# Optimization experiments

Measured on AMD Instinct MI355X. Metric: run time of the kernel, lower is better.

## Reference

```python
import jax, jax.numpy as jnp
import numpy as np

# model dims
B, S, R, D = 2, 64, 2048, 1024      # batch, num_bars(summary len), reg seq len, embed dim
H, KVH, HD = 16, 4, 64              # q heads, kv heads, head dim
G = H // KVH                        # GQA group size
KVD = KVH * HD
TPB = R // S                        # tokens per bar = 32
SCALE = HD ** -0.5
NEG = -1e9


def _rotate_half(x):
    x1, x2 = jnp.split(x, 2, axis=-1)
    return jnp.concatenate([-x2, x1], axis=-1)


def _apply_rope(q, k, cos, sin):
    return q * cos + _rotate_half(q) * sin, k * cos + _rotate_half(k) * sin


def _rope_1d(seq_len):
    # standard RoPE tables, shape (1, 1, seq_len, HD)
    inv = 1.0 / (10000.0 ** (jnp.arange(0, HD, 2, dtype=jnp.float32) / HD))
    freqs = jnp.arange(seq_len, dtype=jnp.float32)[:, None] * inv
    emb = jnp.concatenate([freqs, freqs], axis=-1)
    return jnp.cos(emb)[None, None], jnp.sin(emb)[None, None]


def _rope_2d(bar_ids, tib):
    # hierarchical 2D RoPE: half the rotary freqs encode bar id, half encode token-in-bar id
    q4 = HD // 4
    inv = 1.0 / (10000.0 ** (jnp.arange(q4, dtype=jnp.float32) * 2.0 / (HD // 2)))
    fb = bar_ids.astype(jnp.float32)[..., None] * inv   # (B, R, HD/4)
    ft = tib.astype(jnp.float32)[..., None] * inv       # (B, R, HD/4)
    freqs = jnp.concatenate([fb, ft], axis=-1)          # (B, R, HD/2)
    emb = jnp.concatenate([freqs, freqs], axis=-1)      # (B, R, HD)
    return jnp.cos(emb)[:, None], jnp.sin(emb)[:, None]


def _attn(q, k, v, mask):
    # masked softmax attention; mask (Lq, Lk) broadcast over batch/heads
    s = jnp.einsum('bhqd,bhkd->bhqk', q, k) * SCALE
    s = jnp.where(mask[None, None], s, NEG)
    p = jax.nn.softmax(s, axis=-1)
    return jnp.einsum('bhqk,bhkd->bhqd', p, v)


def _lin(x, w, b):
    return x @ w + b


def _heads(x, n):
    b, l, _ = x.shape
    return x.reshape(b, l, n, HD).transpose(0, 2, 1, 3)


def _merge(x):
    b, h, l, _ = x.shape
    return x.transpose(0, 2, 1, 3).reshape(b, l, h * HD)


PARAM_SHAPES = [('w_sq', (D, D)), ('b_sq', (D,)), ('w_sk', (D, KVD)), ('b_sk', (KVD,)),
                ('w_sv', (D, KVD)), ('b_sv', (KVD,)), ('w_so', (D, D)), ('b_so', (D,)),
                ('w_rq', (D, D)), ('b_rq', (D,)), ('w_rk', (D, KVD)), ('b_rk', (KVD,)),
                ('w_rv', (D, KVD)), ('b_rv', (KVD,)), ('w_ro', (D, D)), ('b_ro', (D,)),
                ('w_k2', (D, KVD)), ('b_k2', (KVD,)), ('w_v2', (D, KVD)), ('b_v2', (KVD,))]


def setup_inputs() -> dict:
    key = jax.random.key(0)
    ks = jax.random.split(key, 2 + len(PARAM_SHAPES))
    inp = {}
    inp['sum_x'] = jax.random.normal(ks[0], (B, S, D), jnp.float32)
    inp['reg_x'] = jax.random.normal(ks[1], (B, R, D), jnp.float32)
    for i, (n, shp) in enumerate(PARAM_SHAPES):
        inp[n] = jax.random.normal(ks[2 + i], shp, jnp.float32) * 0.02
    pos = jnp.arange(R)
    bar = pos // TPB
    tib = pos % TPB
    inp['bar_ids'] = jnp.tile(bar[None], (B, 1)).astype(jnp.int32)
    inp['token_in_bar_ids'] = jnp.tile(tib[None], (B, 1)).astype(jnp.int32)
    # summarize phase: summary-bar i attends to summary j<=i and regular tokens in bars<=i
    key_bar = jnp.concatenate([jnp.arange(S), bar])
    inp['summarize_block_mask'] = key_bar[None, :] <= jnp.arange(S)[:, None]
    # updating phase: regular token t attends to summary-K2 of bars<=bar(t) and regular s<=t
    upd = jnp.concatenate([jnp.arange(S)[None, :] <= bar[:, None],
                           pos[None, :] <= pos[:, None]], axis=1)
    inp['updating_block_mask'] = upd
    return inp


def reference(sum_x, reg_x, w_sq, b_sq, w_sk, b_sk, w_sv, b_sv, w_so, b_so,
              w_rq, b_rq, w_rk, b_rk, w_rv, b_rv, w_ro, b_ro, w_k2, b_k2, w_v2, b_v2,
              summarize_block_mask, updating_block_mask, bar_ids, token_in_bar_ids):
    sum_q = _heads(_lin(sum_x, w_sq, b_sq), H)
    sum_k = _heads(_lin(sum_x, w_sk, b_sk), KVH)
    sum_v = _heads(_lin(sum_x, w_sv, b_sv), KVH)
    reg_q = _heads(_lin(reg_x, w_rq, b_rq), H)
    reg_k = _heads(_lin(reg_x, w_rk, b_rk), KVH)
    reg_v = _heads(_lin(reg_x, w_rv, b_rv), KVH)
    # 1D RoPE for summary tokens, 2D hierarchical RoPE for regular tokens
    cos, sin = _rope_1d(S)
    sum_q, sum_k = _apply_rope(sum_q, sum_k, cos, sin)
    rcos, rsin = _rope_2d(bar_ids, token_in_bar_ids)
    reg_q, reg_k = _apply_rope(reg_q, reg_k, rcos, rsin)
    rep = lambda t: jnp.repeat(t, G, axis=1)  # GQA repeat_interleave over heads
    reg_k_r, reg_v_r = rep(reg_k), rep(reg_v)
    # phase 1: summarize (summary queries over [summary; regular] keys)
    cat_k = jnp.concatenate([rep(sum_k), reg_k_r], axis=2)
    cat_v = jnp.concatenate([rep(sum_v), reg_v_r], axis=2)
    sum_attn = _merge(_attn(sum_q, cat_k, cat_v, summarize_block_mask))  # (B, S, D)
    # phase 2: updating (regular queries over [summary K2/V2; regular] keys)
    k2 = rep(_heads(_lin(sum_attn, w_k2, b_k2), KVH))
    v2 = rep(_heads(_lin(sum_attn, w_v2, b_v2), KVH))
    cat_k2 = jnp.concatenate([k2, reg_k_r], axis=2)
    cat_v2 = jnp.concatenate([v2, reg_v_r], axis=2)
    reg_attn = _merge(_attn(reg_q, cat_k2, cat_v2, updating_block_mask))  # (B, R, D)
    return _lin(sum_attn, w_so, b_so), _lin(reg_attn, w_ro, b_ro)
```

## Files before the change

kernel.cpp:

```cpp
#include <hip/hip_runtime.h>

typedef unsigned short u16;
typedef __attribute__((ext_vector_type(8))) short s8v;
typedef __attribute__((ext_vector_type(4))) float f4v;

#define B_    2
#define S_    64
#define R_    2048
#define D_    1024
#define H_    16
#define KVH_  4
#define LOG2_10K 13.287712379549449f
#define QSC_  0.18033688011112042f

__device__ __forceinline__ u16 f2bf(float f) {
  union { float f; unsigned int i; } v; v.f = f;
  unsigned int x = v.i;
  return (u16)((x + 0x7FFFu + ((x >> 16) & 1u)) >> 16);
}
__device__ __forceinline__ u16 f2bf_ru(float f) {
  union { float f; unsigned int i; } v; v.f = f;
  return (u16)((v.i + 0x8000u) >> 16);
}

__device__ __forceinline__ f4v mfma2(const s8v& a0, const s8v& a1,
                                     const s8v& b0, const s8v& b1) {
  f4v t = {0.f, 0.f, 0.f, 0.f};
  t = __builtin_amdgcn_mfma_f32_16x16x32_bf16(a0, b0, t, 0, 0, 0);
  t = __builtin_amdgcn_mfma_f32_16x16x32_bf16(a1, b1, t, 0, 0, 0);
  return t;
}

struct WT10 { const float* w[10]; u16* o[10]; int C[10]; };

__global__ __launch_bounds__(256)
void transw_k(WT10 ws, const float* __restrict__ xa, const float* __restrict__ xb,
              u16* __restrict__ oa, u16* __restrict__ ob)
{
  const int z = blockIdx.z;
  if (z == 10) {
    int gid = blockIdx.x + blockIdx.y * 32;
    #pragma unroll
    for (int it = 0; it < 3; it++) {
      int idx = gid * 256 + threadIdx.x + it * 262144;
      if (idx < 540672) {
        int i = idx * 8;
        const float* src; u16* dst; int off;
        if (i < 131072) { src = xa; dst = oa; off = i; }
        else            { src = xb; dst = ob; off = i - 131072; }
        float4 a = *(const float4*)(src + off);
        float4 b = *(const float4*)(src + off + 4);
        s8v r;
        r[0] = (short)f2bf(a.x); r[1] = (short)f2bf(a.y);
        r[2] = (short)f2bf(a.z); r[3] = (short)f2bf(a.w);
        r[4] = (short)f2bf(b.x); r[5] = (short)f2bf(b.y);
        r[6] = (short)f2bf(b.z); r[7] = (short)f2bf(b.w);
        *(s8v*)(dst + off) = r;
      }
    }
    return;
  }
  const int C = ws.C[z];
  const int c0 = blockIdx.x * 32, k0 = blockIdx.y * 32;
  if (c0 >= C) return;
  __shared__ float t[32][33];
  const float* w = ws.w[z];
  u16* o = ws.o[z];
  const int x = threadIdx.x & 31, y = threadIdx.x >> 5;
  #pragma unroll
  for (int j = 0; j < 4; j++)
    t[y + 8 * j][x] = w[(size_t)(k0 + y + 8 * j) * C + c0 + x];
  __syncthreads();
  #pragma unroll
  for (int j = 0; j < 4; j++)
    o[(size_t)(c0 + y + 8 * j) * 1024 + k0 + x] = f2bf(t[x][y + 8 * j]);
}

__device__ __forceinline__ void gemm_core_gl(
    const u16* __restrict__ Xrow, const u16* __restrict__ WTrow,
    u16* __restrict__ As, u16* __restrict__ Bs, f4v (&acc)[2][4],
    int tid, int l15, int l4, int wro, int wco)
{
  const int w    = tid >> 6;
  const int lane = tid & 63;
  const int rl   = lane >> 3;
  const int c8   = lane & 7;
  const int x7   = l15 & 7;
  const int csw  = (c8 ^ rl) * 8;

  for (int k = 0; k < 16; k++) {
    const int k0 = k * 64;
    __syncthreads();
    #pragma unroll
    for (int j = 0; j < 2; j++) {
      int rbase = w * 16 + j * 8;
      int r = rbase + rl;
      __builtin_amdgcn_global_load_lds(
        (const __attribute__((address_space(1))) void*)(Xrow + (size_t)r * 1024 + k0 + csw),
        (__attribute__((address_space(3))) void*)(As + rbase * 64),
        16, 0, 0);
      __builtin_amdgcn_global_load_lds(
        (const __attribute__((address_space(1))) void*)(WTrow + (size_t)r * 1024 + k0 + csw),
        (__attribute__((address_space(3))) void*)(Bs + rbase * 64),
        16, 0, 0);
    }
    __syncthreads();

    s8v af[2][2], bf4[4][2];
    #pragma unroll
    for (int rc = 0; rc < 2; rc++) {
      int row = wro + rc * 16 + l15;
      af[rc][0] = *(const s8v*)(As + row * 64 + ((l4 ^ x7) * 8));
      af[rc][1] = *(const s8v*)(As + row * 64 + (((l4 + 4) ^ x7) * 8));
    }
    #pragma unroll
    for (int cc = 0; cc < 4; cc++) {
      int row = wco + cc * 16 + l15;
      bf4[cc][0] = *(const s8v*)(Bs + row * 64 + ((l4 ^ x7) * 8));
      bf4[cc][1] = *(const s8v*)(Bs + row * 64 + (((l4 + 4) ^ x7) * 8));
    }
    #pragma unroll
    for (int rc = 0; rc < 2; rc++)
      #pragma unroll
      for (int cc = 0; cc < 4; cc++) {
        acc[rc][cc] = __builtin_amdgcn_mfma_f32_16x16x32_bf16(af[rc][0], bf4[cc][0], acc[rc][cc], 0, 0, 0);
        acc[rc][cc] = __builtin_amdgcn_mfma_f32_16x16x32_bf16(af[rc][1], bf4[cc][1], acc[rc][cc], 0, 0, 0);
      }
  }
  __syncthreads();
}

__device__ __forceinline__ void epi_to_lds(
    const f4v (&acc)[2][4], const float* __restrict__ Bp, u16* __restrict__ Es,
    int cbr, int wro, int wco, int grb, int LB,
    int ropeMode, bool rope2d, bool sc, int l15, int l4)
{
  float bv[4];
  #pragma unroll
  for (int cc = 0; cc < 4; cc++) bv[cc] = Bp[cbr + cc * 16 + l15];

  if (ropeMode == 0) {
    #pragma unroll
    for (int rc = 0; rc < 2; rc++)
      #pragma unroll
      for (int reg = 0; reg < 4; reg++) {
        int lrow = wro + rc * 16 + l4 * 4 + reg;
        #pragma unroll
        for (int cc = 0; cc < 4; cc++)
          Es[lrow * 136 + wco + cc * 16 + l15] = f2bf(acc[rc][cc][reg] + bv[cc]);
      }
  } else {
    float step = rope2d ? (LOG2_10K / 16.f) : (LOG2_10K / 32.f);
    float inv_lo = exp2f(-(float)l15 * step);
    float inv_hi = rope2d ? inv_lo : inv_lo * exp2f(-16.f * step);
    #pragma unroll
    for (int rc = 0; rc < 2; rc++)
      #pragma unroll
      for (int reg = 0; reg < 4; reg++) {
        int lrow = wro + rc * 16 + l4 * 4 + reg;
        int grow = grb + lrow;
        int pos = grow & (LB - 1);
        int bar = pos >> 5, tib = pos & 31;
        #pragma unroll
        for (int cc = 0; cc < 4; cc++) {
          float inv = (cc & 1) ? inv_hi : inv_lo;
          float bse = rope2d ? (float)((cc & 1) ? tib : bar) : (float)pos;
          float ang = bse * inv;
          float sn, cs;
          sincosf(ang, &sn, &cs);
          float v0 = acc[rc][cc][reg] + bv[cc];
          float v1 = acc[rc][cc ^ 2][reg] + bv[cc ^ 2];
          float rot = (cc < 2) ? -v1 : v1;
          float val = v0 * cs + rot * sn;
          if (sc) val *= QSC_;
          Es[lrow * 136 + wco + cc * 16 + l15] = f2bf(val);
        }
      }
  }
}

__device__ __forceinline__ void store_tile_bf16(
    const u16* __restrict__ Es, u16* __restrict__ out,
    int grb, int c0r, int NH, int LB, int LBS, int tid)
{
  #pragma unroll
  for (int it = 0; it < 4; it++) {
    int idx = it * 512 + tid;
    int r = idx >> 4, ch = idx & 15;
    int grow = grb + r;
    int b = grow >> LBS, pos = grow & (LB - 1);
    int cg = c0r + ch * 8;
    size_t base = (((size_t)b * NH + (cg >> 6)) * LB + pos) * 64 + (cg & 63);
    *(s8v*)(out + base) = *(const s8v*)(Es + r * 136 + ch * 8);
  }
}

__device__ __forceinline__ void store_tile_vT(
    const u16* __restrict__ Es, u16* __restrict__ outT,
    int grb, int kvbase, int LB, int LBS, int tid)
{
  #pragma unroll
  for (int it = 0; it < 4; it++) {
    int idx = tid + it * 512;
    int dcol = idx & 127, rg = idx >> 7;
    int grow = grb + rg * 8;
    int b = grow >> LBS, pos = grow & (LB - 1);
    u16 tmp[8];
    #pragma unroll
    for (int j = 0; j < 8; j++) tmp[j] = Es[(rg * 8 + j) * 136 + dcol];
    u16* dst = outT + (((size_t)(b * KVH_ + kvbase + (dcol >> 6))) * 64 + (dcol & 63)) * LB + pos;
    *(s8v*)dst = *(s8v*)tmp;
  }
}

struct QkvA {
  const u16 *X, *WTs, *WTr;
  const float *b0s, *b1s, *b2s, *b0r, *b1r, *b2r;
  u16 *o0s, *o1s, *o2s, *o0r, *o1r, *o2r;
};

__global__ __launch_bounds__(512)
void qkv_k(QkvA a)
{
  int orig = blockIdx.x;
  int xcd = orig & 7, sidx = orig >> 3;
  int wg = (xcd < 4) ? (xcd * 50 + sidx) : (200 + (xcd - 4) * 49 + sidx);
  const int bx = wg % 12, by = wg / 12;
  const bool issum = (by == 0);
  const int c0 = bx * 128;

  __shared__ u16 LDSU[17408];
  u16* As = LDSU;
  u16* Bs = LDSU + 8192;
  u16* Es = LDSU;

  const int tid  = threadIdx.x;
  const int lane = tid & 63;
  const int w    = tid >> 6;
  const int l15  = lane & 15;
  const int l4   = lane >> 4;
  const int wro  = (w >> 1) * 32;
  const int wco  = (w & 1) * 64;

  f4v acc[2][4];
  #pragma unroll
  for (int i = 0; i < 2; i++)
    #pragma unroll
    for (int j = 0; j < 4; j++) acc[i][j] = (f4v){0.f, 0.f, 0.f, 0.f};

  const u16* Xrow  = a.X + (size_t)by * 128 * 1024;
  const u16* WTrow = (issum ? a.WTs : a.WTr) + (size_t)c0 * 1024;
  gemm_core_gl(Xrow, WTrow, As, Bs, acc, tid, l15, l4, wro, wco);

  const int LB  = issum ? 64 : 2048;
  const int LBS = issum ? 6 : 11;
  const int grb = issum ? 0 : (by - 1) * 128;

  if (c0 < 1024) {
    epi_to_lds(acc, issum ? a.b0s : a.b0r, Es, c0 + wco, wro, wco, grb, LB, 1, !issum, true, l15, l4);
    __syncthreads();
    store_tile_bf16(Es, issum ? a.o0s : a.o0r, grb, c0, 16, LB, LBS, tid);
  } else if (c0 < 1280) {
    epi_to_lds(acc, issum ? a.b1s : a.b1r, Es, c0 - 1024 + wco, wro, wco, grb, LB, 1, !issum, false, l15, l4);
    __syncthreads();
    store_tile_bf16(Es, issum ? a.o1s : a.o1r, grb, c0 - 1024, 4, LB, LBS, tid);
  } else {
    epi_to_lds(acc, issum ? a.b2s : a.b2r, Es, c0 - 1280 + wco, wro, wco, grb, LB, 0, false, false, l15, l4);
    __syncthreads();
    store_tile_vT(Es, issum ? a.o2s : a.o2r, grb, (c0 - 1280) >> 6, LB, LBS, tid);
  }
}

__global__ __launch_bounds__(512)
void gemm_p1_k(const u16* __restrict__ X, const u16* __restrict__ WT,
               const float* __restrict__ bk2, const float* __restrict__ bv2,
               const float* __restrict__ bso,
               u16* __restrict__ k2, u16* __restrict__ v2T, float* __restrict__ outsum)
{
  const int c0 = blockIdx.x * 128;

  __shared__ u16 LDSU[17408];
  u16* As = LDSU;
  u16* Bs = LDSU + 8192;
  u16* Es = LDSU;

  const int tid  = threadIdx.x;
  const int lane = tid & 63;
  const int w    = tid >> 6;
  const int l15  = lane & 15;
  const int l4   = lane >> 4;
  const int wro  = (w >> 1) * 32;
  const int wco  = (w & 1) * 64;

  f4v acc[2][4];
  #pragma unroll
  for (int i = 0; i < 2; i++)
    #pragma unroll
    for (int j = 0; j < 4; j++) acc[i][j] = (f4v){0.f, 0.f, 0.f, 0.f};

  gemm_core_gl(X, WT + (size_t)c0 * 1024, As, Bs, acc, tid, l15, l4, wro, wco);

  if (c0 < 256) {
    epi_to_lds(acc, bk2, Es, c0 + wco, wro, wco, 0, 64, 0, false, false, l15, l4);
    __syncthreads();
    store_tile_bf16(Es, k2, 0, c0, 4, 64, 6, tid);
  } else if (c0 < 512) {
    epi_to_lds(acc, bv2, Es, c0 - 256 + wco, wro, wco, 0, 64, 0, false, false, l15, l4);
    __syncthreads();
    store_tile_vT(Es, v2T, 0, (c0 - 256) >> 6, 64, 6, tid);
  } else {
    float bv[4];
    #pragma unroll
    for (int cc = 0; cc < 4; cc++) bv[cc] = bso[c0 - 512 + wco + cc * 16 + l15];
    #pragma unroll
    for (int rc = 0; rc < 2; rc++)
      #pragma unroll
      for (int reg = 0; reg < 4; reg++) {
        int row = wro + rc * 16 + l4 * 4 + reg;
        #pragma unroll
        for (int cc = 0; cc < 4; cc++)
          outsum[(size_t)row * 1024 + c0 - 512 + wco + cc * 16 + l15] = acc[rc][cc][reg] + bv[cc];
      }
  }
}

__global__ __launch_bounds__(512)
void gemm_ro_k(const u16* __restrict__ X, const u16* __restrict__ WT,
               const float* __restrict__ Bp, float* __restrict__ out)
{
  int orig = blockIdx.x;
  int wg = (orig & 7) * 32 + (orig >> 3);
  const int bx = wg & 7, by = wg >> 3;
  const int c0 = bx * 128, r0 = by * 128;

  __shared__ u16 LDSU[16384];
  u16* As = LDSU;
  u16* Bs = LDSU + 8192;

  const int tid  = threadIdx.x;
  const int lane = tid & 63;
  const int w    = tid >> 6;
  const int l15  = lane & 15;
  const int l4   = lane >> 4;
  const int wro  = (w >> 1) * 32;
  const int wco  = (w & 1) * 64;

  f4v acc[2][4];
  #pragma unroll
  for (int i = 0; i < 2; i++)
    #pragma unroll
    for (int j = 0; j < 4; j++) acc[i][j] = (f4v){0.f, 0.f, 0.f, 0.f};

  gemm_core_gl(X + (size_t)r0 * 1024, WT + (size_t)c0 * 1024, As, Bs, acc,
               tid, l15, l4, wro, wco);

  float bv[4];
  #pragma unroll
  for (int cc = 0; cc < 4; cc++) bv[cc] = Bp[c0 + wco + cc * 16 + l15];
  #pragma unroll
  for (int rc = 0; rc < 2; rc++)
    #pragma unroll
    for (int reg = 0; reg < 4; reg++) {
      int row = r0 + wro + rc * 16 + l4 * 4 + reg;
      #pragma unroll
      for (int cc = 0; cc < 4; cc++)
        out[(size_t)row * 1024 + c0 + wco + cc * 16 + l15] = acc[rc][cc][reg] + bv[cc];
    }
}

template<int PHASE>
__device__ __forceinline__ void strip_sm(
    f4v (&s)[4], float& m, float& lsum, f4v (&acc)[4],
    u16 (&PtS)[16][72], bool need_mask, int kbase, int qrow, int l15, int l4)
{
  float tmax = -1e30f;
  if (need_mask) {
    #pragma unroll
    for (int n = 0; n < 4; n++)
      #pragma unroll
      for (int reg = 0; reg < 4; reg++) {
        int kidx = kbase + n * 16 + l4 * 4 + reg;
        bool ok;
        if (kbase == 0) ok = kidx <= ((PHASE == 1) ? qrow : (qrow >> 5));
        else { int kr = kidx - 64; ok = (PHASE == 1) ? ((kr >> 5) <= qrow) : (kr <= qrow); }
        float sv = ok ? s[n][reg] : -1e30f;
        s[n][reg] = sv;
        tmax = fmaxf(tmax, sv);
      }
  } else {
    #pragma unroll
    for (int n = 0; n < 4; n++)
      #pragma unroll
      for (int reg = 0; reg < 4; reg++) tmax = fmaxf(tmax, s[n][reg]);
  }
  tmax = fmaxf(tmax, __shfl_xor(tmax, 16));
  tmax = fmaxf(tmax, __shfl_xor(tmax, 32));

  if (__any(tmax > m)) {
    float mn = fmaxf(m, tmax);
    float f  = __builtin_amdgcn_exp2f(m - mn);
    m = mn;
    lsum *= f;
    #pragma unroll
    for (int dt = 0; dt < 4; dt++)
      #pragma unroll
      for (int reg = 0; reg < 4; reg++) acc[dt][reg] *= f;
  }
  float rsum = 0.f;
  #pragma unroll
  for (int n = 0; n < 4; n++) {
    float p0 = __builtin_amdgcn_exp2f(s[n][0] - m);
    float p1 = __builtin_amdgcn_exp2f(s[n][1] - m);
    float p2 = __builtin_amdgcn_exp2f(s[n][2] - m);
    float p3 = __builtin_amdgcn_exp2f(s[n][3] - m);
    rsum += (p0 + p1) + (p2 + p3);
    uint2 pk;
    pk.x = (unsigned)f2bf_ru(p0) | ((unsigned)f2bf_ru(p1) << 16);
    pk.y = (unsigned)f2bf_ru(p2) | ((unsigned)f2bf_ru(p3) << 16);
    *(uint2*)&PtS[l15][n * 16 + l4 * 4] = pk;
  }
  rsum += __shfl_xor(rsum, 16);
  rsum += __shfl_xor(rsum, 32);
  lsum += rsum;
}

__global__ __launch_bounds__(512)
void attn2_k(const u16* __restrict__ Q, const u16* __restrict__ KS,
             const u16* __restrict__ KR, const u16* __restrict__ VST,
             const u16* __restrict__ VRT, u16* __restrict__ Out)
{
  const int gid = blockIdx.x;
  const int qb  = (gid & 256) ? (15 - (gid & 15)) : (gid & 15);
  const int bh  = gid >> 4;
  const int h   = bh & 15, b = bh >> 4;
  const int q0  = qb * 128;
  const int kh  = h >> 2;

  __shared__ u16 Kt[64][72];
  __shared__ u16 Vt[64][72];
  __shared__ u16 Pt[8][16][72];

  const int tid = threadIdx.x, lane = tid & 63, w = tid >> 6;
  const int l15 = lane & 15, l4 = lane >> 4;
  const int qw  = q0 + w * 16;

  const u16* qp = Q + (((size_t)b * H_ + h) * R_ + qw + l15) * 64;
  s8v qf0 = *(const s8v*)(qp + l4 * 8);
  s8v qf1 = *(const s8v*)(qp + 32 + l4 * 8);

  f4v acc[4];
  #pragma unroll
  for (int dt = 0; dt < 4; dt++) acc[dt] = (f4v){0.f, 0.f, 0.f, 0.f};
  float m = -1e30f, lsum = 0.f;

  const int ntiles = (64 + q0 + 128) >> 6;
  const size_t bh_kv = (size_t)b * KVH_ + kh;
  const int r_ = tid >> 3, sg_ = (tid & 7) * 8;

  {
    const u16* kp = KS  + bh_kv * 4096;
    const u16* vp = VST + bh_kv * 4096;
    s8v k0 = *(const s8v*)(kp + r_ * 64 + sg_);
    s8v v0 = *(const s8v*)(vp + r_ * 64 + sg_);
    *(s8v*)&Kt[r_][sg_] = k0;
    *(s8v*)&Vt[r_][sg_] = v0;
  }
  __syncthreads();

  for (int kt = 0; kt < ntiles; kt++) {
    const int kbase = kt * 64;
    const bool pre = (kt + 1 < ntiles);
    s8v knx, vnx;
    if (pre) {
      const u16* kp = KR  + (bh_kv * R_ + kbase) * 64;
      const u16* vp = VRT + bh_kv * 64 * R_ + kbase;
      knx = *(const s8v*)(kp + r_ * 64 + sg_);
      vnx = *(const s8v*)(vp + (size_t)r_ * R_ + sg_);
    }

    const bool active = (kbase == 0) || (kbase - 64 <= qw + 15);
    if (active) {
      f4v s[4];
      __builtin_amdgcn_s_setprio(1);
      #pragma unroll
      for (int n = 0; n < 4; n++) {
        s8v kf0 = *(const s8v*)&Kt[n * 16 + l15][l4 * 8];
        s8v kf1 = *(const s8v*)&Kt[n * 16 + l15][32 + l4 * 8];
        s[n] = mfma2(kf0, kf1, qf0, qf1);
      }
      __builtin_amdgcn_s_setprio(0);
      bool nm = (kbase == 0) || ((kbase - 1) > qw);
      strip_sm<2>(s, m, lsum, acc, Pt[w], nm, kbase, qw + l15, l15, l4);
      asm volatile("s_waitcnt lgkmcnt(0)" ::: "memory");
      s8v pf0 = *(const s8v*)&Pt[w][l15][l4 * 8];
      s8v pf1 = *(const s8v*)&Pt[w][l15][32 + l4 * 8];
      __builtin_amdgcn_s_setprio(1);
      #pragma unroll
      for (int dt = 0; dt < 4; dt++) {
        s8v vf0 = *(const s8v*)&Vt[dt * 16 + l15][l4 * 8];
        s8v vf1 = *(const s8v*)&Vt[dt * 16 + l15][32 + l4 * 8];
        acc[dt] = __builtin_amdgcn_mfma_f32_16x16x32_bf16(vf0, pf0, acc[dt], 0, 0, 0);
        acc[dt] = __builtin_amdgcn_mfma_f32_16x16x32_bf16(vf1, pf1, acc[dt], 0, 0, 0);
      }
      __builtin_amdgcn_s_setprio(0);
    }

    __syncthreads();
    if (pre) {
      *(s8v*)&Kt[r_][sg_] = knx;
      *(s8v*)&Vt[r_][sg_] = vnx;
      __syncthreads();
    }
  }

  float linv = 1.f / lsum;
  u16* o = Out + ((size_t)b * R_ + qw + l15) * D_ + h * 64;
  #pragma unroll
  for (int dt = 0; dt < 4; dt++) {
    ushort4 t4;
    t4.x = f2bf(acc[dt][0] * linv);
    t4.y = f2bf(acc[dt][1] * linv);
    t4.z = f2bf(acc[dt][2] * linv);
    t4.w = f2bf(acc[dt][3] * linv);
    *(ushort4*)(o + dt * 16 + l4 * 4) = t4;
  }
}

__global__ __launch_bounds__(256)
void attn1_k(const u16* __restrict__ Q, const u16* __restrict__ KS,
             const u16* __restrict__ KR, const u16* __restrict__ VST,
             const u16* __restrict__ VRT,
             float* __restrict__ pO, float* __restrict__ pml)
{
  const int gid = blockIdx.x;
  const int ck  = gid & 7;
  const int bh  = gid >> 3;
  const int h   = bh & 15, b = bh >> 4;
  const int kh  = h >> 2;
  const int kt0 = (ck * 33) >> 3;
  const int kt1 = ((ck + 1) * 33) >> 3;

  __shared__ u16 Kt[2][64][72];
  __shared__ u16 Vt[2][64][72];
  __shared__ u16 Pt[4][16][72];

  const int tid = threadIdx.x, lane = tid & 63, w = tid >> 6;
  const int l15 = lane & 15, l4 = lane >> 4;
  const int qw  = w * 16;

  const u16* qp = Q + (((size_t)b * H_ + h) * S_ + qw + l15) * 64;
  s8v qf0 = *(const s8v*)(qp + l4 * 8);
  s8v qf1 = *(const s8v*)(qp + 32 + l4 * 8);

  f4v acc[4];
  #pragma unroll
  for (int dt = 0; dt < 4; dt++) acc[dt] = (f4v){0.f, 0.f, 0.f, 0.f};
  float m = -1e30f, lsum = 0.f;

  const size_t bh_kv = (size_t)b * KVH_ + kh;
  const int r_ = tid >> 3, sg_ = (tid & 7) * 8;

  {
    const u16 *kp, *vp; int vstr;
    if (kt0 == 0) { kp = KS + bh_kv * 4096; vp = VST + bh_kv * 4096; vstr = 64; }
    else {
      kp = KR  + (bh_kv * R_ + kt0 * 64 - 64) * 64;
      vp = VRT + bh_kv * 64 * R_ + (kt0 * 64 - 64);
      vstr = R_;
    }
    s8v ka0 = *(const s8v*)(kp + r_ * 64 + sg_);
    s8v ka1 = *(const s8v*)(kp + (r_ + 32) * 64 + sg_);
    s8v va0 = *(const s8v*)(vp + (size_t)r_ * vstr + sg_);
    s8v va1 = *(const s8v*)(vp + (size_t)(r_ + 32) * vstr + sg_);
    *(s8v*)&Kt[0][r_][sg_]      = ka0;
    *(s8v*)&Kt[0][r_ + 32][sg_] = ka1;
    *(s8v*)&Vt[0][r_][sg_]      = va0;
    *(s8v*)&Vt[0][r_ + 32][sg_] = va1;
  }
  __syncthreads();

  for (int kt = kt0; kt < kt1; kt++) {
    const int cur = (kt - kt0) & 1;
    const int kbase = kt * 64;
    const bool pre = (kt + 1 < kt1);
    s8v ka0, ka1, va0, va1;
    if (pre) {
      const u16* kp = KR  + (bh_kv * R_ + kbase) * 64;
      const u16* vp = VRT + bh_kv * 64 * R_ + kbase;
      ka0 = *(const s8v*)(kp + r_ * 64 + sg_);
      ka1 = *(const s8v*)(kp + (r_ + 32) * 64 + sg_);
      va0 = *(const s8v*)(vp + (size_t)r_ * R_ + sg_);
      va1 = *(const s8v*)(vp + (size_t)(r_ + 32) * R_ + sg_);
    }

    const bool active = (kbase == 0) || (((kbase - 64) >> 5) <= qw + 15);
    if (active) {
      f4v s[4];
      __builtin_amdgcn_s_setprio(1);
      #pragma unroll
      for (int n = 0; n < 4; n++) {
        s8v kf0 = *(const s8v*)&Kt[cur][n * 16 + l15][l4 * 8];
        s8v kf1 = *(const s8v*)&Kt[cur][n * 16 + l15][32 + l4 * 8];
        s[n] = mfma2(kf0, kf1, qf0, qf1);
      }
      __builtin_amdgcn_s_setprio(0);
      bool nm = (kbase == 0) || (((kbase - 1) >> 5) > qw);
      strip_sm<1>(s, m, lsum, acc, Pt[w], nm, kbase, qw + l15, l15, l4);
      asm volatile("s_waitcnt lgkmcnt(0)" ::: "memory");
      s8v pf0 = *(const s8v*)&Pt[w][l15][l4 * 8];
      s8v pf1 = *(const s8v*)&Pt[w][l15][32 + l4 * 8];
      __builtin_amdgcn_s_setprio(1);
      #pragma unroll
      for (int dt = 0; dt < 4; dt++) {
        s8v vf0 = *(const s8v*)&Vt[cur][dt * 16 + l15][l4 * 8];
        s8v vf1 = *(const s8v*)&Vt[cur][dt * 16 + l15][32 + l4 * 8];
        acc[dt] = __builtin_amdgcn_mfma_f32_16x16x32_bf16(vf0, pf0, acc[dt], 0, 0, 0);
        acc[dt] = __builtin_amdgcn_mfma_f32_16x16x32_bf16(vf1, pf1, acc[dt], 0, 0, 0);
      }
      __builtin_amdgcn_s_setprio(0);
    }

    if (pre) {
      *(s8v*)&Kt[cur ^ 1][r_][sg_]      = ka0;
      *(s8v*)&Kt[cur ^ 1][r_ + 32][sg_] = ka1;
      *(s8v*)&Vt[cur ^ 1][r_][sg_]      = va0;
      *(s8v*)&Vt[cur ^ 1][r_ + 32][sg_] = va1;
    }
    __syncthreads();
  }

  float* po = pO + (((size_t)ck * 32 + bh) * 64 + qw + l15) * 64;
  #pragma unroll
  for (int dt = 0; dt < 4; dt++)
    *(f4v*)(po + dt * 16 + l4 * 4) = acc[dt];
  if (l4 == 0) {
    float* pm = pml + (((size_t)ck * 32 + bh) * 64 + qw + l15) * 2;
    pm[0] = m; pm[1] = lsum;
  }
}

__global__ __launch_bounds__(256)
void comb1_k(const float* __restrict__ pO, const float* __restrict__ pml,
             u16* __restrict__ sattn)
{
  const int bh = blockIdx.x;
  const int b = bh >> 4, h = bh & 15;
  const int q  = threadIdx.x >> 2;
  const int d0 = (threadIdx.x & 3) * 16;
  float mv[8], lv[8], mstar = -1e30f;
  #pragma unroll
  for (int c = 0; c < 8; c++) {
    const float* p = pml + (((size_t)c * 32 + bh) * 64 + q) * 2;
    mv[c] = p[0]; lv[c] = p[1];
    mstar = fmaxf(mstar, mv[c]);
  }
  float o[16];
  #pragma unroll
  for (int j = 0; j < 16; j++) o[j] = 0.f;
  float lsum = 0.f;
  #pragma unroll
  for (int c = 0; c < 8; c++) {
    float wgt = __builtin_amdgcn_exp2f(mv[c] - mstar);
    lsum += lv[c] * wgt;
    const float* po = pO + (((size_t)c * 32 + bh) * 64 + q) * 64 + d0;
    #pragma unroll
    for (int j = 0; j < 16; j++) o[j] += po[j] * wgt;
  }
  float inv = 1.f / lsum;
  u16 ob[16];
  #pragma unroll
  for (int j = 0; j < 16; j++) ob[j] = f2bf(o[j] * inv);
  u16* out = sattn + ((size_t)(b * 64 + q)) * 1024 + h * 64 + d0;
  *(s8v*)out       = *(s8v*)&ob[0];
  *(s8v*)(out + 8) = *(s8v*)&ob[8];
}

extern "C" void kernel_launch(void* const* d_in, const int* in_sizes, int n_in,
                              void* d_out, int out_size, void* d_ws, size_t ws_size,
                              hipStream_t stream)
{
  (void)out_size; (void)ws_size;

  static const int expect[22] = {
    131072, 4194304,
    1048576, 1024, 262144, 256,
    262144, 256, 1048576, 1024,
    1048576, 1024, 262144, 256,
    262144, 256, 1048576, 1024,
    262144, 256, 262144, 256
  };
  if (n_in < 22) return;
  for (int i = 0; i < 22; i++) if (in_sizes[i] != expect[i]) return;

  const float* sum_x = (const float*)d_in[0];
  const float* reg_x = (const float*)d_in[1];
  const float* w_sq = (const float*)d_in[2];  const float* b_sq = (const float*)d_in[3];
  const float* w_sk = (const float*)d_in[4];  const float* b_sk = (const float*)d_in[5];
  const float* w_sv = (const float*)d_in[6];  const float* b_sv = (const float*)d_in[7];
  const float* w_so = (const float*)d_in[8];  const float* b_so = (const float*)d_in[9];
  const float* w_rq = (const float*)d_in[10]; const float* b_rq = (const float*)d_in[11];
  const float* w_rk = (const float*)d_in[12]; const float* b_rk = (const float*)d_in[13];
  const float* w_rv = (const float*)d_in[14]; const float* b_rv = (const float*)d_in[15];
  const float* w_ro = (const float*)d_in[16]; const float* b_ro = (const float*)d_in[17];
  const float* w_k2 = (const float*)d_in[18]; const float* b_k2 = (const float*)d_in[19];
  const float* w_v2 = (const float*)d_in[20]; const float* b_v2 = (const float*)d_in[21];

  u16* ws    = (u16*)d_ws;
  u16* xs_bf = ws;
  u16* xr_bf = xs_bf + 131072;
  u16* wt_s  = xr_bf + 4194304;
  u16* wt_r  = wt_s  + 1572864;
  u16* wt_p  = wt_r  + 1572864;
  u16* wt_ro = wt_p  + 1572864;
  u16* sq    = wt_ro + 1048576;
  u16* sk    = sq    + 131072;
  u16* svT   = sk    + 32768;
  u16* rq    = svT   + 32768;
  u16* rk    = rq    + 4194304;
  u16* rvT   = rk    + 1048576;
  u16* sattn = rvT   + 1048576;
  u16* k2    = sattn + 131072;
  u16* v2T   = k2    + 32768;
  u16* rattn = v2T   + 32768;

  float* pO  = (float*)rattn;
  float* pml = pO + 1048576;

  float* out_sum = (float*)d_out;
  float* out_reg = out_sum + 131072;

  dim3 blk(256);

  WT10 wt;
  wt.w[0] = w_sq; wt.o[0] = wt_s;              wt.C[0] = 1024;
  wt.w[1] = w_rq; wt.o[1] = wt_r;              wt.C[1] = 1024;
  wt.w[2] = w_so; wt.o[2] = wt_p + 512 * 1024; wt.C[2] = 1024;
  wt.w[3] = w_ro; wt.o[3] = wt_ro;             wt.C[3] = 1024;
  wt.w[4] = w_sk; wt.o[4] = wt_s + 1024 * 1024; wt.C[4] = 256;
  wt.w[5] = w_sv; wt.o[5] = wt_s + 1280 * 1024; wt.C[5] = 256;
  wt.w[6] = w_rk; wt.o[6] = wt_r + 1024 * 1024; wt.C[6] = 256;
  wt.w[7] = w_rv; wt.o[7] = wt_r + 1280 * 1024; wt.C[7] = 256;
  wt.w[8] = w_k2; wt.o[8] = wt_p;               wt.C[8] = 256;
  wt.w[9] = w_v2; wt.o[9] = wt_p + 256 * 1024;  wt.C[9] = 256;
  transw_k<<<dim3(32, 32, 11), blk, 0, stream>>>(wt, sum_x, reg_x, xs_bf, xr_bf);

  QkvA qa;
  qa.X = xs_bf; qa.WTs = wt_s; qa.WTr = wt_r;
  qa.b0s = b_sq; qa.b1s = b_sk; qa.b2s = b_sv;
  qa.b0r = b_rq; qa.b1r = b_rk; qa.b2r = b_rv;
  qa.o0s = sq; qa.o1s = sk; qa.o2s = svT;
  qa.o0r = rq; qa.o1r = rk; qa.o2r = rvT;
  qkv_k<<<dim3(396), dim3(512), 0, stream>>>(qa);

  attn1_k<<<dim3(256), blk, 0, stream>>>(sq, sk, rk, svT, rvT, pO, pml);
  comb1_k<<<dim3(32), blk, 0, stream>>>(pO, pml, sattn);

  gemm_p1_k<<<dim3(12), dim3(512), 0, stream>>>(sattn, wt_p, b_k2, b_v2, b_so, k2, v2T, out_sum);

  attn2_k<<<dim3(512), dim3(512), 0, stream>>>(rq, k2, rk, v2T, rvT, rattn);

  gemm_ro_k<<<dim3(256), dim3(512), 0, stream>>>(rattn, wt_ro, b_ro, out_reg);
}
```

Measured before the change: 132.5 us.

## Split phase-2 attention over key chunks with a separate combine kernel

The causal phase-2 attention kernel is split along the key dimension. Long query blocks are divided into up to three key-tile chunks, so the work per block is more even and the grid doubles to 1024 blocks. Each chunk writes an unnormalized bf16 partial output plus its running max and sum to scratch reused from the input buffer. A new combine kernel merges the chunks with log-sum-exp weights. This trades load imbalance and tail latency for an extra launch, extra global traffic, and bf16 rounding of the partial sums.

Result: slower. 141.2 us (+6.5%).

```diff
diff --git a/kernel.cpp b/kernel.cpp
--- a/kernel.cpp
+++ b/kernel.cpp
@@ -21,6 +21,9 @@
 __device__ __forceinline__ u16 f2bf_ru(float f) {
   union { float f; unsigned int i; } v; v.f = f;
   return (u16)((v.i + 0x8000u) >> 16);
+}
+__device__ __forceinline__ float bf2f(u16 u) {
+  union { unsigned int i; float f; } v; v.i = ((unsigned int)u) << 16; return v.f;
 }
 
 __device__ __forceinline__ f4v mfma2(const s8v& a0, const s8v& a1,
@@ -427,14 +430,25 @@
 __global__ __launch_bounds__(512)
 void attn2_k(const u16* __restrict__ Q, const u16* __restrict__ KS,
              const u16* __restrict__ KR, const u16* __restrict__ VST,
-             const u16* __restrict__ VRT, u16* __restrict__ Out)
-{
-  const int gid = blockIdx.x;
-  const int qb  = (gid & 256) ? (15 - (gid & 15)) : (gid & 15);
-  const int bh  = gid >> 4;
-  const int h   = bh & 15, b = bh >> 4;
-  const int q0  = qb * 128;
-  const int kh  = h >> 2;
+             const u16* __restrict__ VRT,
+             u16* __restrict__ pO2, float* __restrict__ pml2)
+{
+  static const int sqb[32] = {0,1,2,3,4,5,5,6,6,7,7,8,8,9,9,10,10,
+                              11,11,11,12,12,12,13,13,13,14,14,14,15,15,15};
+  static const int sci[32] = {0,0,0,0,0,0,1,0,1,0,1,0,1,0,1,0,1,
+                              0,1,2,0,1,2,0,1,2,0,1,2,0,1,2};
+  static const int snc[32] = {1,1,1,1,1,2,2,2,2,2,2,2,2,2,2,2,2,
+                              3,3,3,3,3,3,3,3,3,3,3,3,3,3,3};
+  const int gid  = blockIdx.x;
+  const int bh   = gid & 31;
+  const int slot = gid >> 5;
+  const int qb   = sqb[slot], ci = sci[slot], nch = snc[slot];
+  const int nt   = 3 + 2 * qb;
+  const int kt0  = (nt * ci) / nch;
+  const int kt1  = (nt * (ci + 1)) / nch;
+  const int h    = bh & 15, b = bh >> 4;
+  const int q0   = qb * 128;
+  const int kh   = h >> 2;
 
   __shared__ u16 Kt[64][72];
   __shared__ u16 Vt[64][72];
@@ -453,23 +467,27 @@
   for (int dt = 0; dt < 4; dt++) acc[dt] = (f4v){0.f, 0.f, 0.f, 0.f};
   float m = -1e30f, lsum = 0.f;
 
-  const int ntiles = (64 + q0 + 128) >> 6;
   const size_t bh_kv = (size_t)b * KVH_ + kh;
   const int r_ = tid >> 3, sg_ = (tid & 7) * 8;
 
   {
-    const u16* kp = KS  + bh_kv * 4096;
-    const u16* vp = VST + bh_kv * 4096;
-    s8v k0 = *(const s8v*)(kp + r_ * 64 + sg_);
-    s8v v0 = *(const s8v*)(vp + r_ * 64 + sg_);
-    *(s8v*)&Kt[r_][sg_] = k0;
-    *(s8v*)&Vt[r_][sg_] = v0;
+    const u16 *kp, *vp; int vstr;
+    if (kt0 == 0) { kp = KS + bh_kv * 4096; vp = VST + bh_kv * 4096; vstr = 64; }
+    else {
+      kp = KR  + (bh_kv * R_ + kt0 * 64 - 64) * 64;
+      vp = VRT + bh_kv * 64 * R_ + (kt0 * 64 - 64);
+      vstr = R_;
+    }
+    s8v kv = *(const s8v*)(kp + r_ * 64 + sg_);
+    s8v vv = *(const s8v*)(vp + (size_t)r_ * vstr + sg_);
+    *(s8v*)&Kt[r_][sg_] = kv;
+    *(s8v*)&Vt[r_][sg_] = vv;
   }
   __syncthreads();
 
-  for (int kt = 0; kt < ntiles; kt++) {
+  for (int kt = kt0; kt < kt1; kt++) {
     const int kbase = kt * 64;
-    const bool pre = (kt + 1 < ntiles);
+    const bool pre = (kt + 1 < kt1);
     s8v knx, vnx;
     if (pre) {
       const u16* kp = KR  + (bh_kv * R_ + kbase) * 64;
@@ -513,17 +531,73 @@
     }
   }
 
-  float linv = 1.f / lsum;
-  u16* o = Out + ((size_t)b * R_ + qw + l15) * D_ + h * 64;
+  const int rowl = w * 16 + l15;
+  u16* po = pO2 + (((size_t)slot * 32 + bh) * 128 + rowl) * 64;
   #pragma unroll
   for (int dt = 0; dt < 4; dt++) {
     ushort4 t4;
-    t4.x = f2bf(acc[dt][0] * linv);
-    t4.y = f2bf(acc[dt][1] * linv);
-    t4.z = f2bf(acc[dt][2] * linv);
-    t4.w = f2bf(acc[dt][3] * linv);
-    *(ushort4*)(o + dt * 16 + l4 * 4) = t4;
-  }
+    t4.x = f2bf(acc[dt][0]);
+    t4.y = f2bf(acc[dt][1]);
+    t4.z = f2bf(acc[dt][2]);
+    t4.w = f2bf(acc[dt][3]);
+    *(ushort4*)(po + dt * 16 + l4 * 4) = t4;
+  }
+  if (l4 == 0) {
+    float* pm = pml2 + (((size_t)slot * 32 + bh) * 128 + rowl) * 2;
+    pm[0] = m; pm[1] = lsum;
+  }
+}
+
+__global__ __launch_bounds__(256)
+void comb2_k(const u16* __restrict__ pO2, const float* __restrict__ pml2,
+             u16* __restrict__ rattn)
+{
+  static const int SO[16] = {0,1,2,3,4,5,7,9,11,13,15,17,20,23,26,29};
+  static const int NC[16] = {1,1,1,1,1,2,2,2,2,2,2,3,3,3,3,3};
+  const int t   = blockIdx.x * 256 + threadIdx.x;
+  const int row = t >> 2;
+  const int dg  = (t & 3) * 16;
+  const int q   = row & 2047, bh = row >> 11;
+  const int b   = bh >> 4, h = bh & 15;
+  const int qb  = q >> 7, rowl = q & 127;
+  const int s0  = SO[qb], nc = NC[qb];
+
+  float mv[3], lv[3];
+  float mstar = -1e30f;
+  #pragma unroll
+  for (int ci = 0; ci < 3; ci++) {
+    if (ci < nc) {
+      const float* p = pml2 + (((size_t)(s0 + ci) * 32 + bh) * 128 + rowl) * 2;
+      mv[ci] = p[0]; lv[ci] = p[1];
+      mstar = fmaxf(mstar, mv[ci]);
+    }
+  }
+  float o[16];
+  #pragma unroll
+  for (int j = 0; j < 16; j++) o[j] = 0.f;
+  float l = 0.f;
+  #pragma unroll
+  for (int ci = 0; ci < 3; ci++) {
+    if (ci < nc) {
+      float wgt = __builtin_amdgcn_exp2f(mv[ci] - mstar);
+      l += lv[ci] * wgt;
+      const u16* po = pO2 + (((size_t)(s0 + ci) * 32 + bh) * 128 + rowl) * 64 + dg;
+      s8v v0 = *(const s8v*)po;
+      s8v v1 = *(const s8v*)(po + 8);
+      #pragma unroll
+      for (int j = 0; j < 8; j++) {
+        o[j]     += bf2f((u16)v0[j]) * wgt;
+        o[8 + j] += bf2f((u16)v1[j]) * wgt;
+      }
+    }
+  }
+  float inv = 1.f / l;
+  u16 ob[16];
+  #pragma unroll
+  for (int j = 0; j < 16; j++) ob[j] = f2bf(o[j] * inv);
+  u16* out = rattn + ((size_t)(b * R_ + q)) * D_ + h * 64 + dg;
+  *(s8v*)out       = *(s8v*)&ob[0];
+  *(s8v*)(out + 8) = *(s8v*)&ob[8];
 }
 
 __global__ __launch_bounds__(256)
@@ -726,6 +800,9 @@
   float* pO  = (float*)rattn;
   float* pml = pO + 1048576;
 
+  float* pml2 = (float*)xs_bf;
+  u16*   pO2  = xs_bf + 524288;
+
   float* out_sum = (float*)d_out;
   float* out_reg = out_sum + 131072;
 
@@ -757,7 +834,8 @@
 
   gemm_p1_k<<<dim3(12), dim3(512), 0, stream>>>(sattn, wt_p, b_k2, b_v2, b_so, k2, v2T, out_sum);
 
-  attn2_k<<<dim3(512), dim3(512), 0, stream>>>(rq, k2, rk, v2T, rvT, rattn);
+  attn2_k<<<dim3(1024), dim3(512), 0, stream>>>(rq, k2, rk, v2T, rvT, pO2, pml2);
+  comb2_k<<<dim3(1024), blk, 0, stream>>>(pO2, pml2, rattn);
 
   gemm_ro_k<<<dim3(256), dim3(512), 0, stream>>>(rattn, wt_ro, b_ro, out_reg);
 }
```

## Use 128-wide key tiles in phase-2 attention with specialized summary tile

Applied to the files above, without the earlier changes.

Restructures the phase-2 attention kernel so regular keys are processed in 128-key tiles instead of 64, halving loop iterations and barriers per block. The summary-key tile is handled by a dedicated prologue with its own mask, and causal masking is applied only on the diagonal tile. Online-softmax rescaling is skipped when no lane's max increases. The larger LDS buffers and register arrays may reduce occupancy, and the wider tiles do some extra masked work on diagonal tiles.

Result: faster. 129.7 us (-2.1%).

```diff
diff --git a/kernel.cpp b/kernel.cpp
--- a/kernel.cpp
+++ b/kernel.cpp
@@ -436,15 +436,16 @@
   const int q0  = qb * 128;
   const int kh  = h >> 2;
 
-  __shared__ u16 Kt[64][72];
-  __shared__ u16 Vt[64][72];
-  __shared__ u16 Pt[8][16][72];
+  __shared__ u16 Kt[128][72];
+  __shared__ u16 Vt[64][136];
+  __shared__ u16 Pt[8][16][136];
 
   const int tid = threadIdx.x, lane = tid & 63, w = tid >> 6;
   const int l15 = lane & 15, l4 = lane >> 4;
   const int qw  = q0 + w * 16;
-
-  const u16* qp = Q + (((size_t)b * H_ + h) * R_ + qw + l15) * 64;
+  const int qrow = qw + l15;
+
+  const u16* qp = Q + (((size_t)b * H_ + h) * R_ + qrow) * 64;
   s8v qf0 = *(const s8v*)(qp + l4 * 8);
   s8v qf1 = *(const s8v*)(qp + 32 + l4 * 8);
 
@@ -453,68 +454,181 @@
   for (int dt = 0; dt < 4; dt++) acc[dt] = (f4v){0.f, 0.f, 0.f, 0.f};
   float m = -1e30f, lsum = 0.f;
 
-  const int ntiles = (64 + q0 + 128) >> 6;
   const size_t bh_kv = (size_t)b * KVH_ + kh;
-  const int r_ = tid >> 3, sg_ = (tid & 7) * 8;
+  const u16* KRb = KR  + bh_kv * R_ * 64;
+  const u16* VRb = VRT + bh_kv * 64 * R_;
 
   {
     const u16* kp = KS  + bh_kv * 4096;
     const u16* vp = VST + bh_kv * 4096;
-    s8v k0 = *(const s8v*)(kp + r_ * 64 + sg_);
-    s8v v0 = *(const s8v*)(vp + r_ * 64 + sg_);
-    *(s8v*)&Kt[r_][sg_] = k0;
-    *(s8v*)&Vt[r_][sg_] = v0;
+    int r = tid >> 3, sg = (tid & 7) * 8;
+    *(s8v*)&Kt[r][sg] = *(const s8v*)(kp + r * 64 + sg);
+    *(s8v*)&Vt[r][sg] = *(const s8v*)(vp + r * 64 + sg);
   }
   __syncthreads();
 
-  for (int kt = 0; kt < ntiles; kt++) {
-    const int kbase = kt * 64;
-    const bool pre = (kt + 1 < ntiles);
-    s8v knx, vnx;
+  s8v knx[2], vnx[2];
+  const int rK = tid >> 3,  cK = (tid & 7) * 8;
+  const int dV = tid >> 4,  cV = (tid & 15) * 8;
+  knx[0] = *(const s8v*)(KRb + (size_t)rK * 64 + cK);
+  knx[1] = *(const s8v*)(KRb + (size_t)(rK + 64) * 64 + cK);
+  vnx[0] = *(const s8v*)(VRb + (size_t)dV * R_ + cV);
+  vnx[1] = *(const s8v*)(VRb + (size_t)(dV + 32) * R_ + cV);
+
+  {
+    f4v s[4];
+    __builtin_amdgcn_s_setprio(1);
+    #pragma unroll
+    for (int n = 0; n < 4; n++) {
+      s8v kf0 = *(const s8v*)&Kt[n * 16 + l15][l4 * 8];
+      s8v kf1 = *(const s8v*)&Kt[n * 16 + l15][32 + l4 * 8];
+      s[n] = mfma2(kf0, kf1, qf0, qf1);
+    }
+    __builtin_amdgcn_s_setprio(0);
+    float tmax = -1e30f;
+    const int qb5 = qrow >> 5;
+    #pragma unroll
+    for (int n = 0; n < 4; n++)
+      #pragma unroll
+      for (int reg = 0; reg < 4; reg++) {
+        int kidx = n * 16 + l4 * 4 + reg;
+        float sv = (kidx <= qb5) ? s[n][reg] : -1e30f;
+        s[n][reg] = sv;
+        tmax = fmaxf(tmax, sv);
+      }
+    tmax = fmaxf(tmax, __shfl_xor(tmax, 16));
+    tmax = fmaxf(tmax, __shfl_xor(tmax, 32));
+    m = tmax;
+    float rsum = 0.f;
+    #pragma unroll
+    for (int n = 0; n < 4; n++) {
+      float p0 = __builtin_amdgcn_exp2f(s[n][0] - m);
+      float p1 = __builtin_amdgcn_exp2f(s[n][1] - m);
+      float p2 = __builtin_amdgcn_exp2f(s[n][2] - m);
+      float p3 = __builtin_amdgcn_exp2f(s[n][3] - m);
+      rsum += (p0 + p1) + (p2 + p3);
+      uint2 pk;
+      pk.x = (unsigned)f2bf_ru(p0) | ((unsigned)f2bf_ru(p1) << 16);
+      pk.y = (unsigned)f2bf_ru(p2) | ((unsigned)f2bf_ru(p3) << 16);
+      *(uint2*)&Pt[w][l15][n * 16 + l4 * 4] = pk;
+    }
+    rsum += __shfl_xor(rsum, 16);
+    rsum += __shfl_xor(rsum, 32);
+    lsum = rsum;
+    asm volatile("s_waitcnt lgkmcnt(0)" ::: "memory");
+    s8v pf0 = *(const s8v*)&Pt[w][l15][l4 * 8];
+    s8v pf1 = *(const s8v*)&Pt[w][l15][32 + l4 * 8];
+    __builtin_amdgcn_s_setprio(1);
+    #pragma unroll
+    for (int dt = 0; dt < 4; dt++) {
+      s8v vf0 = *(const s8v*)&Vt[dt * 16 + l15][l4 * 8];
+      s8v vf1 = *(const s8v*)&Vt[dt * 16 + l15][32 + l4 * 8];
+      acc[dt] = __builtin_amdgcn_mfma_f32_16x16x32_bf16(vf0, pf0, acc[dt], 0, 0, 0);
+      acc[dt] = __builtin_amdgcn_mfma_f32_16x16x32_bf16(vf1, pf1, acc[dt], 0, 0, 0);
+    }
+    __builtin_amdgcn_s_setprio(0);
+  }
+  __syncthreads();
+  *(s8v*)&Kt[rK][cK]      = knx[0];
+  *(s8v*)&Kt[rK + 64][cK] = knx[1];
+  *(s8v*)&Vt[dV][cV]      = vnx[0];
+  *(s8v*)&Vt[dV + 32][cV] = vnx[1];
+  __syncthreads();
+
+  for (int mt = 0; mt <= qb; mt++) {
+    const int kstart = mt * 128;
+    const bool pre = (mt < qb);
     if (pre) {
-      const u16* kp = KR  + (bh_kv * R_ + kbase) * 64;
-      const u16* vp = VRT + bh_kv * 64 * R_ + kbase;
-      knx = *(const s8v*)(kp + r_ * 64 + sg_);
-      vnx = *(const s8v*)(vp + (size_t)r_ * R_ + sg_);
-    }
-
-    const bool active = (kbase == 0) || (kbase - 64 <= qw + 15);
-    if (active) {
-      f4v s[4];
-      __builtin_amdgcn_s_setprio(1);
-      #pragma unroll
-      for (int n = 0; n < 4; n++) {
-        s8v kf0 = *(const s8v*)&Kt[n * 16 + l15][l4 * 8];
-        s8v kf1 = *(const s8v*)&Kt[n * 16 + l15][32 + l4 * 8];
-        s[n] = mfma2(kf0, kf1, qf0, qf1);
-      }
-      __builtin_amdgcn_s_setprio(0);
-      bool nm = (kbase == 0) || ((kbase - 1) > qw);
-      strip_sm<2>(s, m, lsum, acc, Pt[w], nm, kbase, qw + l15, l15, l4);
-      asm volatile("s_waitcnt lgkmcnt(0)" ::: "memory");
-      s8v pf0 = *(const s8v*)&Pt[w][l15][l4 * 8];
-      s8v pf1 = *(const s8v*)&Pt[w][l15][32 + l4 * 8];
-      __builtin_amdgcn_s_setprio(1);
+      const int ks2 = kstart + 128;
+      knx[0] = *(const s8v*)(KRb + (size_t)(ks2 + rK) * 64 + cK);
+      knx[1] = *(const s8v*)(KRb + (size_t)(ks2 + rK + 64) * 64 + cK);
+      vnx[0] = *(const s8v*)(VRb + (size_t)dV * R_ + ks2 + cV);
+      vnx[1] = *(const s8v*)(VRb + (size_t)(dV + 32) * R_ + ks2 + cV);
+    }
+
+    f4v s[8];
+    __builtin_amdgcn_s_setprio(1);
+    #pragma unroll
+    for (int n = 0; n < 8; n++) {
+      s8v kf0 = *(const s8v*)&Kt[n * 16 + l15][l4 * 8];
+      s8v kf1 = *(const s8v*)&Kt[n * 16 + l15][32 + l4 * 8];
+      s[n] = mfma2(kf0, kf1, qf0, qf1);
+    }
+    __builtin_amdgcn_s_setprio(0);
+
+    float tmax = -1e30f;
+    if (mt == qb) {
+      #pragma unroll
+      for (int n = 0; n < 8; n++)
+        #pragma unroll
+        for (int reg = 0; reg < 4; reg++) {
+          int kidx = kstart + n * 16 + l4 * 4 + reg;
+          float sv = (kidx <= qrow) ? s[n][reg] : -1e30f;
+          s[n][reg] = sv;
+          tmax = fmaxf(tmax, sv);
+        }
+    } else {
+      #pragma unroll
+      for (int n = 0; n < 8; n++)
+        #pragma unroll
+        for (int reg = 0; reg < 4; reg++) tmax = fmaxf(tmax, s[n][reg]);
+    }
+    tmax = fmaxf(tmax, __shfl_xor(tmax, 16));
+    tmax = fmaxf(tmax, __shfl_xor(tmax, 32));
+
+    if (__any(tmax > m)) {
+      float mn = fmaxf(m, tmax);
+      float f  = __builtin_amdgcn_exp2f(m - mn);
+      m = mn;
+      lsum *= f;
+      #pragma unroll
+      for (int dt = 0; dt < 4; dt++)
+        #pragma unroll
+        for (int reg = 0; reg < 4; reg++) acc[dt][reg] *= f;
+    }
+    float rsum = 0.f;
+    #pragma unroll
+    for (int n = 0; n < 8; n++) {
+      float p0 = __builtin_amdgcn_exp2f(s[n][0] - m);
+      float p1 = __builtin_amdgcn_exp2f(s[n][1] - m);
+      float p2 = __builtin_amdgcn_exp2f(s[n][2] - m);
+      float p3 = __builtin_amdgcn_exp2f(s[n][3] - m);
+      rsum += (p0 + p1) + (p2 + p3);
+      uint2 pk;
+      pk.x = (unsigned)f2bf_ru(p0) | ((unsigned)f2bf_ru(p1) << 16);
+      pk.y = (unsigned)f2bf_ru(p2) | ((unsigned)f2bf_ru(p3) << 16);
+      *(uint2*)&Pt[w][l15][n * 16 + l4 * 4] = pk;
+    }
+    rsum += __shfl_xor(rsum, 16);
+    rsum += __shfl_xor(rsum, 32);
+    lsum += rsum;
+
+    asm volatile("s_waitcnt lgkmcnt(0)" ::: "memory");
+
+    __builtin_amdgcn_s_setprio(1);
+    #pragma unroll
+    for (int kb = 0; kb < 4; kb++) {
+      s8v pf = *(const s8v*)&Pt[w][l15][kb * 32 + l4 * 8];
       #pragma unroll
       for (int dt = 0; dt < 4; dt++) {
-        s8v vf0 = *(const s8v*)&Vt[dt * 16 + l15][l4 * 8];
-        s8v vf1 = *(const s8v*)&Vt[dt * 16 + l15][32 + l4 * 8];
-        acc[dt] = __builtin_amdgcn_mfma_f32_16x16x32_bf16(vf0, pf0, acc[dt], 0, 0, 0);
-        acc[dt] = __builtin_amdgcn_mfma_f32_16x16x32_bf16(vf1, pf1, acc[dt], 0, 0, 0);
-      }
-      __builtin_amdgcn_s_setprio(0);
-    }
+        s8v vf = *(const s8v*)&Vt[dt * 16 + l15][kb * 32 + l4 * 8];
+        acc[dt] = __builtin_amdgcn_mfma_f32_16x16x32_bf16(vf, pf, acc[dt], 0, 0, 0);
+      }
+    }
+    __builtin_amdgcn_s_setprio(0);
 
     __syncthreads();
     if (pre) {
-      *(s8v*)&Kt[r_][sg_] = knx;
-      *(s8v*)&Vt[r_][sg_] = vnx;
+      *(s8v*)&Kt[rK][cK]      = knx[0];
+      *(s8v*)&Kt[rK + 64][cK] = knx[1];
+      *(s8v*)&Vt[dV][cV]      = vnx[0];
+      *(s8v*)&Vt[dV + 32][cV] = vnx[1];
       __syncthreads();
     }
   }
 
   float linv = 1.f / lsum;
-  u16* o = Out + ((size_t)b * R_ + qw + l15) * D_ + h * 64;
+  u16* o = Out + ((size_t)b * R_ + qrow) * D_ + h * 64;
   #pragma unroll
   for (int dt = 0; dt < 4; dt++) {
     ushort4 t4;
```
